# Kernel tuning notes

Measured on AMD Instinct MI355X. Metric: run time of the kernel, lower is better.

Reference implementation:

```python
import jax, jax.numpy as jnp
import numpy as np

N_CRD = 32   # ceil(0.5 * 64) coordinate features
K = 16       # clus_val for knn
EPS = 1e-12


def _masked_dist(coords, mask):
    """Pairwise euclidean distances with padded/self pairs set to +inf.
    coords: [B,N,D], mask: [B,N] bool. Returns dist [B,N,N], valid [B,N,N]."""
    sq = jnp.sum(coords * coords, axis=-1)                 # [B,N]
    gram = jnp.einsum('bnd,bmd->bnm', coords, coords)      # [B,N,N]
    d2 = sq[:, :, None] + sq[:, None, :] - 2.0 * gram
    dist = jnp.sqrt(jnp.clip(d2, EPS, None))
    eye = jnp.eye(dist.shape[-1], dtype=bool)
    valid = (mask[:, :, None] & mask[:, None, :]) & ~eye   # fc adjmat, no self-loops
    dist = jnp.where(valid, dist, jnp.inf)                 # pad_val = +inf for eucl
    return dist, valid


def _knn(dist, k):
    """Boolean adjacency: True for the k smallest distances per row."""
    _, idx = jax.lax.top_k(-dist, k)                       # [B,N,K] nearest neighbours
    B, N, _ = dist.shape
    b = jnp.arange(B)[:, None, None]
    n = jnp.arange(N)[None, :, None]
    return jnp.zeros((B, N, N), bool).at[b, n, idx].set(True)


def setup_inputs() -> dict:
    key = jax.random.key(0)
    k1, k2 = jax.random.split(key)
    B, N, F = 64, 1024, 64
    nodes = jax.random.normal(k1, (B, N, F), jnp.float32)
    # realistic ragged graphs: each graph has between N/2 and N valid nodes
    lengths = jax.random.randint(k2, (B,), N // 2, N + 1)
    mask = jnp.arange(N)[None, :] < lengths[:, None]       # [B,N] bool
    return {"nodes": nodes, "mask": mask}


def reference(nodes, mask):
    coords = nodes[..., :N_CRD]
    dist, valid = _masked_dist(coords, mask)
    adjmat = _knn(dist, K) & valid                         # drop padded/self picks
    # dense analogue of distmat[new_adjmat].unsqueeze(-1): zeros off the adjacency
    new_edges = jnp.where(adjmat[..., None], dist[..., None], 0.0)  # [B,N,N,1]
    return new_edges, adjmat
```

## Files before the change

### kernel.cpp

```cpp
#include <hip/hip_runtime.h>
#include <math.h>

#define NROW 1024
#define INF_BITS 0x7F800000u
#define WINDOW   4.0e-3f
#define CLAMP_EPS 1e-12f

typedef float nf4 __attribute__((ext_vector_type(4)));

__device__ __forceinline__ unsigned long long ull_min(unsigned long long a, unsigned long long b) {
    return a < b ? a : b;
}
__device__ __forceinline__ unsigned umax2(unsigned a, unsigned b) { return a > b ? a : b; }

#define ROW_MINMAX(K, MN, MX)                                                           \
    {                                                                                   \
        MN = 0xFFFFFFFFu; MX = 0u;                                                      \
        _Pragma("unroll")                                                               \
        for (int tt = 0; tt < 16; ++tt) {                                               \
            const unsigned kk_ = K[tt];                                                 \
            MN = kk_ < MN ? kk_ : MN;                                                   \
            const unsigned kf_ = (kk_ < INF_BITS) ? kk_ : 0u;                           \
            MX = kf_ > MX ? kf_ : MX;                                                   \
        }                                                                               \
        _Pragma("unroll")                                                               \
        for (int d = 1; d < 64; d <<= 1) {                                              \
            const unsigned omn = (unsigned)__shfl_xor((int)MN, d);                      \
            const unsigned omx = (unsigned)__shfl_xor((int)MX, d);                      \
            MN = omn < MN ? omn : MN;                                                   \
            MX = omx > MX ? omx : MX;                                                   \
        }                                                                               \
    }

#define BISECT_STEP(K, LO, HI)                                                          \
    {                                                                                   \
        const unsigned mid_ = LO + ((HI - LO) >> 1);                                    \
        int cnt_ = 0;                                                                   \
        _Pragma("unroll")                                                               \
        for (int tt = 0; tt < 16; ++tt)                                                 \
            cnt_ += __popcll(__ballot(K[tt] < mid_));                                   \
        if (cnt_ >= 16) HI = mid_; else LO = mid_;                                      \
    }

#define RESOLVE_ROW(K, V, RLOC, SELOUT)                                                 \
    {                                                                                   \
        const float Vw = __uint_as_float(V) + WINDOW;                                   \
        int cS = 0, nE = 0, cW = 0;                                                     \
        unsigned ltm = 0u, eqm = 0u, cm = 0u;                                           \
        _Pragma("unroll")                                                               \
        for (int tt = 0; tt < 16; ++tt) {                                               \
            const unsigned kk_ = K[tt];                                                 \
            const bool l_ = kk_ < (V);                                                  \
            const bool e_ = kk_ == (V);                                                 \
            const bool c_ = __uint_as_float(kk_) <= Vw;                                 \
            cS += __popcll(__ballot(l_));                                               \
            nE += __popcll(__ballot(e_));                                               \
            cW += __popcll(__ballot(c_));                                               \
            ltm |= (l_ ? 1u : 0u) << tt;                                                \
            eqm |= (e_ ? 1u : 0u) << tt;                                                \
            cm  |= (c_ ? 1u : 0u) << tt;                                                \
        }                                                                               \
        if (cS + nE == 16 && cW == 16) {                                                \
            SELOUT = ltm | eqm;                                                         \
        } else {                                                                        \
            int myj = -1;                                                               \
            {                                                                           \
                int cum = 0;                                                            \
                _Pragma("unroll")                                                       \
                for (int tt = 0; tt < 16; ++tt) {                                       \
                    const unsigned long long bm = __ballot((cm >> tt) & 1u);            \
                    const int pc = __popcll(bm);                                        \
                    if (myj < 0 && lane >= cum && lane < cum + pc) {                    \
                        unsigned long long mm = bm;                                     \
                        for (int z = lane - cum; z > 0; --z) mm &= mm - 1ull;           \
                        myj = tt * 64 + (__ffsll((unsigned long long)mm) - 1);          \
                    }                                                                   \
                    cum += pc;                                                          \
                }                                                                       \
            }                                                                           \
            unsigned long long dbits = ~0ull;                                           \
            if (myj >= 0) {                                                             \
                const float4* cp = (const float4*)(nbase + (size_t)myj * 64);           \
                double sq_ = 0.0, dt_ = 0.0;                                            \
                _Pragma("unroll")                                                       \
                for (int f = 0; f < 8; ++f) {                                           \
                    const float4 v = cp[f];                                             \
                    const float4 a = rowc[(RLOC) * 8 + f];                              \
                    sq_ = fma((double)v.x, (double)v.x, sq_);                           \
                    sq_ = fma((double)v.y, (double)v.y, sq_);                           \
                    sq_ = fma((double)v.z, (double)v.z, sq_);                           \
                    sq_ = fma((double)v.w, (double)v.w, sq_);                           \
                    dt_ = fma((double)v.x, (double)a.x, dt_);                           \
                    dt_ = fma((double)v.y, (double)a.y, dt_);                           \
                    dt_ = fma((double)v.z, (double)a.z, dt_);                           \
                    dt_ = fma((double)v.w, (double)a.w, dt_);                           \
                }                                                                       \
                double d64 = fma(-2.0, dt_, sqr64[RLOC] + sq_);                         \
                d64 = fmax(d64, (double)CLAMP_EPS);                                     \
                dbits = (unsigned long long)__double_as_longlong(d64);                  \
            }                                                                           \
            unsigned selb = 0u;                                                         \
            bool act = (myj >= 0);                                                      \
            for (int round = 0; round < 16; ++round) {                                  \
                unsigned long long best = act ? dbits : ~0ull;                          \
                _Pragma("unroll")                                                       \
                for (int d = 1; d < 64; d <<= 1)                                        \
                    best = ull_min(best,                                                \
                        (unsigned long long)__shfl_xor((long long)best, d));            \
                int pj = (act && dbits == best) ? myj : 0x7FFFFFFF;                     \
                _Pragma("unroll")                                                       \
                for (int d = 1; d < 64; d <<= 1) {                                      \
                    const int o = __shfl_xor(pj, d);                                    \
                    pj = o < pj ? o : pj;                                               \
                }                                                                       \
                if (myj == pj) act = false;                                             \
                if (lane == (pj & 63)) selb |= 1u << (pj >> 6);                         \
            }                                                                           \
            SELOUT = selb;                                                              \
        }                                                                               \
    }

__global__ __launch_bounds__(256) void transpose_norm_kernel(
    const float* __restrict__ nodes, float4* __restrict__ wsT,
    float* __restrict__ sqc)
{
    const int w = blockIdx.x;
    const int l = (w & 7) * 32 + (w >> 3);
    const int g = l * 256 + threadIdx.x;
    const int b = g >> 10, j = g & 1023;
    const float4* cp = (const float4*)(nodes + (size_t)g * 64);
    float4 c[8];
    float s = 0.f;
#pragma unroll
    for (int f = 0; f < 8; ++f) {
        c[f] = cp[f];
        s = fmaf(c[f].x, c[f].x, s); s = fmaf(c[f].y, c[f].y, s);
        s = fmaf(c[f].z, c[f].z, s); s = fmaf(c[f].w, c[f].w, s);
    }
#pragma unroll
    for (int f = 0; f < 8; ++f)
        wsT[(((size_t)b * 8 + f) << 10) + j] = c[f];
    sqc[g] = s;
}

template <int USE_WS>
__global__ __launch_bounds__(64) void edge_knn_kernel(
    const float* __restrict__ nodes,
    const int*   __restrict__ mask,
    const float4* __restrict__ wsT,
    const float* __restrict__ sqcw,
    float*       __restrict__ out)
{
    const int lane = threadIdx.x;
    const int blk  = (int)((blockIdx.x & 7) * 2048 + (blockIdx.x >> 3));
    const int b    = blk >> 8;
    const int rowbase = (blk & 255) * 4;

    const int* maskb = mask + b * NROW;
    float* edges = out + (size_t)b * NROW * NROW;
    float* adjm  = out + (size_t)64 * NROW * NROW + (size_t)b * NROW * NROW;

    const int anyv = maskb[rowbase] | maskb[rowbase + 1] | maskb[rowbase + 2] | maskb[rowbase + 3];
    if (!anyv) {
        const nf4 z = {0.f, 0.f, 0.f, 0.f};
#pragma unroll
        for (int r = 0; r < 4; ++r) {
            nf4* e4 = reinterpret_cast<nf4*>(edges + (size_t)(rowbase + r) * NROW);
            nf4* a4 = reinterpret_cast<nf4*>(adjm  + (size_t)(rowbase + r) * NROW);
#pragma unroll
            for (int q = 0; q < 4; ++q) {
                __builtin_nontemporal_store(z, e4 + q * 64 + lane);
                __builtin_nontemporal_store(z, a4 + q * 64 + lane);
            }
        }
        return;
    }

    __shared__ float4 rowc[4 * 8];
    __shared__ float  sqr32s[4];
    __shared__ double sqr64[4];

    const float* nbase = nodes + (size_t)b * NROW * 64;

    if (lane < 32) {
        const int r = lane >> 3, f = lane & 7;
        rowc[lane] = ((const float4*)(nbase + (size_t)(rowbase + r) * 64))[f];
    }
    __syncthreads();
    if (lane < 4) {
        double s = 0.0;
#pragma unroll
        for (int f = 0; f < 8; ++f) {
            const float4 v = rowc[lane * 8 + f];
            s = fma((double)v.x, (double)v.x, s);
            s = fma((double)v.y, (double)v.y, s);
            s = fma((double)v.z, (double)v.z, s);
            s = fma((double)v.w, (double)v.w, s);
        }
        sqr64[lane] = s;
        sqr32s[lane] = (float)s;
    }
    __syncthreads();

    unsigned mb = 0u;
#pragma unroll
    for (int tt = 0; tt < 16; ++tt)
        mb |= (maskb[tt * 64 + lane] != 0 ? 1u : 0u) << tt;

    const int row0 = rowbase;
    const bool rv0 = maskb[row0 + 0] != 0;
    const bool rv1 = maskb[row0 + 1] != 0;
    const bool rv2 = maskb[row0 + 2] != 0;
    const bool rv3 = maskb[row0 + 3] != 0;
    const float sqr0 = sqr32s[0], sqr1 = sqr32s[1];
    const float sqr2 = sqr32s[2], sqr3 = sqr32s[3];

    unsigned k0[16], k1[16], k2[16], k3[16];

#pragma unroll
    for (int tt = 0; tt < 16; ++tt) {
        if (__ballot((mb >> tt) & 1u) == 0ull) {
            k0[tt] = INF_BITS; k1[tt] = INF_BITS;
            k2[tt] = INF_BITS; k3[tt] = INF_BITS;
            continue;
        }
        const int j = tt * 64 + lane;
        float4 c[8];
        float sA;
        if (USE_WS) {
            const float4* tbase = wsT + ((size_t)b * 8 << 10);
#pragma unroll
            for (int f = 0; f < 8; ++f) c[f] = tbase[(f << 10) + j];
            sA = sqcw[(size_t)b * NROW + j];
        } else {
            const float4* cp = (const float4*)(nbase + (size_t)j * 64);
#pragma unroll
            for (int f = 0; f < 8; ++f) c[f] = cp[f];
            sA = 0.f;
#pragma unroll
            for (int f = 0; f < 8; ++f) {
                sA = fmaf(c[f].x, c[f].x, sA); sA = fmaf(c[f].y, c[f].y, sA);
                sA = fmaf(c[f].z, c[f].z, sA); sA = fmaf(c[f].w, c[f].w, sA);
            }
        }

        float d0 = 0.f, d1 = 0.f, d2 = 0.f, d3 = 0.f;
#pragma unroll
        for (int f = 0; f < 8; ++f) {
            const float4 v  = c[f];
            const float4 a0 = rowc[0 * 8 + f];
            const float4 a1 = rowc[1 * 8 + f];
            const float4 a2 = rowc[2 * 8 + f];
            const float4 a3 = rowc[3 * 8 + f];
            d0 = fmaf(v.x, a0.x, d0); d0 = fmaf(v.y, a0.y, d0);
            d0 = fmaf(v.z, a0.z, d0); d0 = fmaf(v.w, a0.w, d0);
            d1 = fmaf(v.x, a1.x, d1); d1 = fmaf(v.y, a1.y, d1);
            d1 = fmaf(v.z, a1.z, d1); d1 = fmaf(v.w, a1.w, d1);
            d2 = fmaf(v.x, a2.x, d2); d2 = fmaf(v.y, a2.y, d2);
            d2 = fmaf(v.z, a2.z, d2); d2 = fmaf(v.w, a2.w, d2);
            d3 = fmaf(v.x, a3.x, d3); d3 = fmaf(v.y, a3.y, d3);
            d3 = fmaf(v.z, a3.z, d3); d3 = fmaf(v.w, a3.w, d3);
        }

        const bool cv = (mb >> tt) & 1u;
        float e_;
        e_ = fmaxf(fmaf(-2.f, d0, sqr0 + sA), CLAMP_EPS);
        k0[tt] = (cv && j != row0 + 0) ? __float_as_uint(e_) : INF_BITS;
        e_ = fmaxf(fmaf(-2.f, d1, sqr1 + sA), CLAMP_EPS);
        k1[tt] = (cv && j != row0 + 1) ? __float_as_uint(e_) : INF_BITS;
        e_ = fmaxf(fmaf(-2.f, d2, sqr2 + sA), CLAMP_EPS);
        k2[tt] = (cv && j != row0 + 2) ? __float_as_uint(e_) : INF_BITS;
        e_ = fmaxf(fmaf(-2.f, d3, sqr3 + sA), CLAMP_EPS);
        k3[tt] = (cv && j != row0 + 3) ? __float_as_uint(e_) : INF_BITS;
    }

    unsigned mn0, mx0, mn1, mx1, mn2, mx2, mn3, mx3;
    ROW_MINMAX(k0, mn0, mx0);
    ROW_MINMAX(k1, mn1, mx1);
    ROW_MINMAX(k2, mn2, mx2);
    ROW_MINMAX(k3, mn3, mx3);

    unsigned lo0 = mn0, hi0 = mx0 + 1u;
    unsigned lo1 = mn1, hi1 = mx1 + 1u;
    unsigned lo2 = mn2, hi2 = mx2 + 1u;
    unsigned lo3 = mn3, hi3 = mx3 + 1u;
    if (!rv0) { lo0 = 0u; hi0 = 1u; }
    if (!rv1) { lo1 = 0u; hi1 = 1u; }
    if (!rv2) { lo2 = 0u; hi2 = 1u; }
    if (!rv3) { lo3 = 0u; hi3 = 1u; }

    for (;;) {
        const unsigned dm = umax2(umax2(hi0 - lo0, hi1 - lo1), umax2(hi2 - lo2, hi3 - lo3));
        if (dm <= 1u) break;
        BISECT_STEP(k0, lo0, hi0);
        BISECT_STEP(k1, lo1, hi1);
        BISECT_STEP(k2, lo2, hi2);
        BISECT_STEP(k3, lo3, hi3);
    }

    unsigned sel0 = 0u, sel1 = 0u, sel2 = 0u, sel3 = 0u;
    if (rv0) RESOLVE_ROW(k0, lo0, 0, sel0);
    if (rv1) RESOLVE_ROW(k1, lo1, 1, sel1);
    if (rv2) RESOLVE_ROW(k2, lo2, 2, sel2);
    if (rv3) RESOLVE_ROW(k3, lo3, 3, sel3);

#pragma unroll
    for (int tt = 0; tt < 16; ++tt) {
        const int j = tt * 64 + lane;
        {
            const bool s = (sel0 >> tt) & 1u;
            edges[(size_t)(row0 + 0) * NROW + j] = s ? sqrtf(__uint_as_float(k0[tt])) : 0.f;
            adjm [(size_t)(row0 + 0) * NROW + j] = s ? 1.f : 0.f;
        }
        {
            const bool s = (sel1 >> tt) & 1u;
            edges[(size_t)(row0 + 1) * NROW + j] = s ? sqrtf(__uint_as_float(k1[tt])) : 0.f;
            adjm [(size_t)(row0 + 1) * NROW + j] = s ? 1.f : 0.f;
        }
        {
            const bool s = (sel2 >> tt) & 1u;
            edges[(size_t)(row0 + 2) * NROW + j] = s ? sqrtf(__uint_as_float(k2[tt])) : 0.f;
            adjm [(size_t)(row0 + 2) * NROW + j] = s ? 1.f : 0.f;
        }
        {
            const bool s = (sel3 >> tt) & 1u;
            edges[(size_t)(row0 + 3) * NROW + j] = s ? sqrtf(__uint_as_float(k3[tt])) : 0.f;
            adjm [(size_t)(row0 + 3) * NROW + j] = s ? 1.f : 0.f;
        }
    }
}

extern "C" void kernel_launch(void* const* d_in, const int* in_sizes, int n_in,
                              void* d_out, int out_size, void* d_ws, size_t ws_size,
                              hipStream_t stream)
{
    const float* nodes = (const float*)d_in[0];
    const int*   mask  = (const int*)d_in[1];
    float* out = (float*)d_out;

    dim3 grid(64 * 256);
    dim3 block(64);

    const size_t wsT_f4 = (size_t)64 * 8 * 1024;
    const size_t need   = wsT_f4 * sizeof(float4) + (size_t)64 * NROW * sizeof(float);
    const bool   use_ws = ws_size >= need;

    if (use_ws) {
        float4* wsT = (float4*)d_ws;
        float*  sqc = (float*)((char*)d_ws + wsT_f4 * sizeof(float4));
        hipLaunchKernelGGL(transpose_norm_kernel, dim3(64 * NROW / 256), dim3(256), 0, stream,
                           nodes, wsT, sqc);
        hipLaunchKernelGGL((edge_knn_kernel<1>), grid, block, 0, stream,
                           nodes, mask, (const float4*)wsT, (const float*)sqc, out);
    } else {
        hipLaunchKernelGGL((edge_knn_kernel<0>), grid, block, 0, stream,
                           nodes, mask, (const float4*)nullptr, (const float*)nullptr, out);
    }
}
```

Baseline: 265.8 us.

## Process eight rows per wavefront and use nontemporal stores for outputs

Each single-wavefront block now handles eight query rows instead of four, halving the grid and reusing each loaded column tile across twice as many dot products. This cuts the repeated column loads from the transposed workspace. Output stores become nontemporal. The price is twice the register state for keys (128 unsigned per lane), which may lower occupancy or spill, and the bisection loop now runs until the slowest of eight rows converges.

After: 351.0 us. +32.1%, slower.

```diff
diff --git a/kernel.cpp b/kernel.cpp
--- a/kernel.cpp
+++ b/kernel.cpp
@@ -120,6 +120,25 @@
         }                                                                               \
     }
 
+#define DOT1(V, A, D)                                                                   \
+    D = fmaf(V.x, A.x, D); D = fmaf(V.y, A.y, D);                                       \
+    D = fmaf(V.z, A.z, D); D = fmaf(V.w, A.w, D);
+
+#define MK(K, D, SQR, RIDX)                                                             \
+    {                                                                                   \
+        const float e_ = fmaxf(fmaf(-2.f, D, (SQR) + sA), CLAMP_EPS);                   \
+        K[tt] = (cv && j != row0 + (RIDX)) ? __float_as_uint(e_) : INF_BITS;            \
+    }
+
+#define ST(K, SEL, RIDX)                                                                \
+    {                                                                                   \
+        const bool s = ((SEL) >> tt) & 1u;                                              \
+        __builtin_nontemporal_store(s ? sqrtf(__uint_as_float(K[tt])) : 0.f,            \
+                                    edges + (size_t)(row0 + (RIDX)) * NROW + j);        \
+        __builtin_nontemporal_store(s ? 1.f : 0.f,                                      \
+                                    adjm + (size_t)(row0 + (RIDX)) * NROW + j);         \
+    }
+
 __global__ __launch_bounds__(256) void transpose_norm_kernel(
     const float* __restrict__ nodes, float4* __restrict__ wsT,
     float* __restrict__ sqc)
@@ -152,42 +171,44 @@
     float*       __restrict__ out)
 {
     const int lane = threadIdx.x;
-    const int blk  = (int)((blockIdx.x & 7) * 2048 + (blockIdx.x >> 3));
-    const int b    = blk >> 8;
-    const int rowbase = (blk & 255) * 4;
+    const int blk  = (int)((blockIdx.x & 7) * 1024 + (blockIdx.x >> 3));
+    const int b    = blk >> 7;
+    const int rowbase = (blk & 127) * 8;
 
     const int* maskb = mask + b * NROW;
     float* edges = out + (size_t)b * NROW * NROW;
     float* adjm  = out + (size_t)64 * NROW * NROW + (size_t)b * NROW * NROW;
 
-    const int anyv = maskb[rowbase] | maskb[rowbase + 1] | maskb[rowbase + 2] | maskb[rowbase + 3];
+    int anyv = 0;
+#pragma unroll
+    for (int r = 0; r < 8; ++r) anyv |= maskb[rowbase + r];
     if (!anyv) {
         const nf4 z = {0.f, 0.f, 0.f, 0.f};
 #pragma unroll
-        for (int r = 0; r < 4; ++r) {
+        for (int r = 0; r < 8; ++r) {
             nf4* e4 = reinterpret_cast<nf4*>(edges + (size_t)(rowbase + r) * NROW);
             nf4* a4 = reinterpret_cast<nf4*>(adjm  + (size_t)(rowbase + r) * NROW);
 #pragma unroll
-            for (int q = 0; q < 4; ++q) {
-                __builtin_nontemporal_store(z, e4 + q * 64 + lane);
-                __builtin_nontemporal_store(z, a4 + q * 64 + lane);
+            for (int p = 0; p < 4; ++p) {
+                __builtin_nontemporal_store(z, e4 + p * 64 + lane);
+                __builtin_nontemporal_store(z, a4 + p * 64 + lane);
             }
         }
         return;
     }
 
-    __shared__ float4 rowc[4 * 8];
-    __shared__ float  sqr32s[4];
-    __shared__ double sqr64[4];
+    __shared__ float4 rowc[8 * 8];
+    __shared__ float  sqr32s[8];
+    __shared__ double sqr64[8];
 
     const float* nbase = nodes + (size_t)b * NROW * 64;
 
-    if (lane < 32) {
+    {
         const int r = lane >> 3, f = lane & 7;
         rowc[lane] = ((const float4*)(nbase + (size_t)(rowbase + r) * 64))[f];
     }
     __syncthreads();
-    if (lane < 4) {
+    if (lane < 8) {
         double s = 0.0;
 #pragma unroll
         for (int f = 0; f < 8; ++f) {
@@ -212,16 +233,20 @@
     const bool rv1 = maskb[row0 + 1] != 0;
     const bool rv2 = maskb[row0 + 2] != 0;
     const bool rv3 = maskb[row0 + 3] != 0;
-    const float sqr0 = sqr32s[0], sqr1 = sqr32s[1];
-    const float sqr2 = sqr32s[2], sqr3 = sqr32s[3];
-
-    unsigned k0[16], k1[16], k2[16], k3[16];
+    const bool rv4 = maskb[row0 + 4] != 0;
+    const bool rv5 = maskb[row0 + 5] != 0;
+    const bool rv6 = maskb[row0 + 6] != 0;
+    const bool rv7 = maskb[row0 + 7] != 0;
+    const float sqr0 = sqr32s[0], sqr1 = sqr32s[1], sqr2 = sqr32s[2], sqr3 = sqr32s[3];
+    const float sqr4 = sqr32s[4], sqr5 = sqr32s[5], sqr6 = sqr32s[6], sqr7 = sqr32s[7];
+
+    unsigned k0[16], k1[16], k2[16], k3[16], k4[16], k5[16], k6[16], k7[16];
 
 #pragma unroll
     for (int tt = 0; tt < 16; ++tt) {
         if (__ballot((mb >> tt) & 1u) == 0ull) {
-            k0[tt] = INF_BITS; k1[tt] = INF_BITS;
-            k2[tt] = INF_BITS; k3[tt] = INF_BITS;
+            k0[tt] = INF_BITS; k1[tt] = INF_BITS; k2[tt] = INF_BITS; k3[tt] = INF_BITS;
+            k4[tt] = INF_BITS; k5[tt] = INF_BITS; k6[tt] = INF_BITS; k7[tt] = INF_BITS;
             continue;
         }
         const int j = tt * 64 + lane;
@@ -245,6 +270,7 @@
         }
 
         float d0 = 0.f, d1 = 0.f, d2 = 0.f, d3 = 0.f;
+        float d4 = 0.f, d5 = 0.f, d6 = 0.f, d7 = 0.f;
 #pragma unroll
         for (int f = 0; f < 8; ++f) {
             const float4 v  = c[f];
@@ -252,81 +278,66 @@
             const float4 a1 = rowc[1 * 8 + f];
             const float4 a2 = rowc[2 * 8 + f];
             const float4 a3 = rowc[3 * 8 + f];
-            d0 = fmaf(v.x, a0.x, d0); d0 = fmaf(v.y, a0.y, d0);
-            d0 = fmaf(v.z, a0.z, d0); d0 = fmaf(v.w, a0.w, d0);
-            d1 = fmaf(v.x, a1.x, d1); d1 = fmaf(v.y, a1.y, d1);
-            d1 = fmaf(v.z, a1.z, d1); d1 = fmaf(v.w, a1.w, d1);
-            d2 = fmaf(v.x, a2.x, d2); d2 = fmaf(v.y, a2.y, d2);
-            d2 = fmaf(v.z, a2.z, d2); d2 = fmaf(v.w, a2.w, d2);
-            d3 = fmaf(v.x, a3.x, d3); d3 = fmaf(v.y, a3.y, d3);
-            d3 = fmaf(v.z, a3.z, d3); d3 = fmaf(v.w, a3.w, d3);
+            const float4 a4 = rowc[4 * 8 + f];
+            const float4 a5 = rowc[5 * 8 + f];
+            const float4 a6 = rowc[6 * 8 + f];
+            const float4 a7 = rowc[7 * 8 + f];
+            DOT1(v, a0, d0); DOT1(v, a1, d1); DOT1(v, a2, d2); DOT1(v, a3, d3);
+            DOT1(v, a4, d4); DOT1(v, a5, d5); DOT1(v, a6, d6); DOT1(v, a7, d7);
         }
 
         const bool cv = (mb >> tt) & 1u;
-        float e_;
-        e_ = fmaxf(fmaf(-2.f, d0, sqr0 + sA), CLAMP_EPS);
-        k0[tt] = (cv && j != row0 + 0) ? __float_as_uint(e_) : INF_BITS;
-        e_ = fmaxf(fmaf(-2.f, d1, sqr1 + sA), CLAMP_EPS);
-        k1[tt] = (cv && j != row0 + 1) ? __float_as_uint(e_) : INF_BITS;
-        e_ = fmaxf(fmaf(-2.f, d2, sqr2 + sA), CLAMP_EPS);
-        k2[tt] = (cv && j != row0 + 2) ? __float_as_uint(e_) : INF_BITS;
-        e_ = fmaxf(fmaf(-2.f, d3, sqr3 + sA), CLAMP_EPS);
-        k3[tt] = (cv && j != row0 + 3) ? __float_as_uint(e_) : INF_BITS;
+        MK(k0, d0, sqr0, 0); MK(k1, d1, sqr1, 1); MK(k2, d2, sqr2, 2); MK(k3, d3, sqr3, 3);
+        MK(k4, d4, sqr4, 4); MK(k5, d5, sqr5, 5); MK(k6, d6, sqr6, 6); MK(k7, d7, sqr7, 7);
     }
 
     unsigned mn0, mx0, mn1, mx1, mn2, mx2, mn3, mx3;
-    ROW_MINMAX(k0, mn0, mx0);
-    ROW_MINMAX(k1, mn1, mx1);
-    ROW_MINMAX(k2, mn2, mx2);
-    ROW_MINMAX(k3, mn3, mx3);
-
-    unsigned lo0 = mn0, hi0 = mx0 + 1u;
-    unsigned lo1 = mn1, hi1 = mx1 + 1u;
-    unsigned lo2 = mn2, hi2 = mx2 + 1u;
-    unsigned lo3 = mn3, hi3 = mx3 + 1u;
+    unsigned mn4, mx4, mn5, mx5, mn6, mx6, mn7, mx7;
+    ROW_MINMAX(k0, mn0, mx0); ROW_MINMAX(k1, mn1, mx1);
+    ROW_MINMAX(k2, mn2, mx2); ROW_MINMAX(k3, mn3, mx3);
+    ROW_MINMAX(k4, mn4, mx4); ROW_MINMAX(k5, mn5, mx5);
+    ROW_MINMAX(k6, mn6, mx6); ROW_MINMAX(k7, mn7, mx7);
+
+    unsigned lo0 = mn0, hi0 = mx0 + 1u, lo1 = mn1, hi1 = mx1 + 1u;
+    unsigned lo2 = mn2, hi2 = mx2 + 1u, lo3 = mn3, hi3 = mx3 + 1u;
+    unsigned lo4 = mn4, hi4 = mx4 + 1u, lo5 = mn5, hi5 = mx5 + 1u;
+    unsigned lo6 = mn6, hi6 = mx6 + 1u, lo7 = mn7, hi7 = mx7 + 1u;
     if (!rv0) { lo0 = 0u; hi0 = 1u; }
     if (!rv1) { lo1 = 0u; hi1 = 1u; }
     if (!rv2) { lo2 = 0u; hi2 = 1u; }
     if (!rv3) { lo3 = 0u; hi3 = 1u; }
+    if (!rv4) { lo4 = 0u; hi4 = 1u; }
+    if (!rv5) { lo5 = 0u; hi5 = 1u; }
+    if (!rv6) { lo6 = 0u; hi6 = 1u; }
+    if (!rv7) { lo7 = 0u; hi7 = 1u; }
 
     for (;;) {
-        const unsigned dm = umax2(umax2(hi0 - lo0, hi1 - lo1), umax2(hi2 - lo2, hi3 - lo3));
+        const unsigned dm = umax2(
+            umax2(umax2(hi0 - lo0, hi1 - lo1), umax2(hi2 - lo2, hi3 - lo3)),
+            umax2(umax2(hi4 - lo4, hi5 - lo5), umax2(hi6 - lo6, hi7 - lo7)));
         if (dm <= 1u) break;
-        BISECT_STEP(k0, lo0, hi0);
-        BISECT_STEP(k1, lo1, hi1);
-        BISECT_STEP(k2, lo2, hi2);
-        BISECT_STEP(k3, lo3, hi3);
+        BISECT_STEP(k0, lo0, hi0); BISECT_STEP(k1, lo1, hi1);
+        BISECT_STEP(k2, lo2, hi2); BISECT_STEP(k3, lo3, hi3);
+        BISECT_STEP(k4, lo4, hi4); BISECT_STEP(k5, lo5, hi5);
+        BISECT_STEP(k6, lo6, hi6); BISECT_STEP(k7, lo7, hi7);
     }
 
     unsigned sel0 = 0u, sel1 = 0u, sel2 = 0u, sel3 = 0u;
+    unsigned sel4 = 0u, sel5 = 0u, sel6 = 0u, sel7 = 0u;
     if (rv0) RESOLVE_ROW(k0, lo0, 0, sel0);
     if (rv1) RESOLVE_ROW(k1, lo1, 1, sel1);
     if (rv2) RESOLVE_ROW(k2, lo2, 2, sel2);
     if (rv3) RESOLVE_ROW(k3, lo3, 3, sel3);
+    if (rv4) RESOLVE_ROW(k4, lo4, 4, sel4);
+    if (rv5) RESOLVE_ROW(k5, lo5, 5, sel5);
+    if (rv6) RESOLVE_ROW(k6, lo6, 6, sel6);
+    if (rv7) RESOLVE_ROW(k7, lo7, 7, sel7);
 
 #pragma unroll
     for (int tt = 0; tt < 16; ++tt) {
         const int j = tt * 64 + lane;
-        {
-            const bool s = (sel0 >> tt) & 1u;
-            edges[(size_t)(row0 + 0) * NROW + j] = s ? sqrtf(__uint_as_float(k0[tt])) : 0.f;
-            adjm [(size_t)(row0 + 0) * NROW + j] = s ? 1.f : 0.f;
-        }
-        {
-            const bool s = (sel1 >> tt) & 1u;
-            edges[(size_t)(row0 + 1) * NROW + j] = s ? sqrtf(__uint_as_float(k1[tt])) : 0.f;
-            adjm [(size_t)(row0 + 1) * NROW + j] = s ? 1.f : 0.f;
-        }
-        {
-            const bool s = (sel2 >> tt) & 1u;
-            edges[(size_t)(row0 + 2) * NROW + j] = s ? sqrtf(__uint_as_float(k2[tt])) : 0.f;
-            adjm [(size_t)(row0 + 2) * NROW + j] = s ? 1.f : 0.f;
-        }
-        {
-            const bool s = (sel3 >> tt) & 1u;
-            edges[(size_t)(row0 + 3) * NROW + j] = s ? sqrtf(__uint_as_float(k3[tt])) : 0.f;
-            adjm [(size_t)(row0 + 3) * NROW + j] = s ? 1.f : 0.f;
-        }
+        ST(k0, sel0, 0); ST(k1, sel1, 1); ST(k2, sel2, 2); ST(k3, sel3, 3);
+        ST(k4, sel4, 4); ST(k5, sel5, 5); ST(k6, sel6, 6); ST(k7, sel7, 7);
     }
 }
 
@@ -338,7 +349,7 @@
     const int*   mask  = (const int*)d_in[1];
     float* out = (float*)d_out;
 
-    dim3 grid(64 * 256);
+    dim3 grid(64 * 128);
     dim3 block(64);
 
     const size_t wsT_f4 = (size_t)64 * 8 * 1024;
```
